# Kernel tuning notes

Hardware: AMD Instinct MI355X
Metric: run time of the kernel (lower is better)

## Reference

```python
import jax, jax.numpy as jnp
import numpy as np

N_NODES = 100000
N_EDGES = 600000
IN_FEATS = 128
HIDDEN = 128


def sage_conv(x, src, dst, w_l, b_l, w_r, num_nodes):
    """PyG SAGEConv with mean aggregation.
    out = mean_{j in N(i)} x_j @ w_l.T + b_l + x_i @ w_r.T
    src/dst: int arrays [E]; messages flow src -> dst.
    """
    msgs = x[src]                                             # [E, F] gather
    summed = jax.ops.segment_sum(msgs, dst, num_segments=num_nodes)  # [N, F]
    ones = jnp.ones((src.shape[0],), dtype=x.dtype)
    deg = jax.ops.segment_sum(ones, dst, num_segments=num_nodes)     # [N]
    agg = summed / jnp.maximum(deg, 1.0)[:, None]             # mean, safe for deg=0
    return agg @ w_l.T + b_l + x @ w_r.T


def setup_inputs() -> dict:
    key = jax.random.key(0)
    ks = jax.random.split(key, 10)

    def glorot(k, shape):
        fan_in = shape[-1]
        bound = 1.0 / np.sqrt(fan_in)
        return jax.random.uniform(k, shape, jnp.float32, -bound, bound)

    x = jax.random.normal(ks[0], (N_NODES, IN_FEATS), dtype=jnp.float32)
    xedge = jax.random.randint(ks[1], (2, N_EDGES), 0, N_NODES, dtype=jnp.int64)
    return {
        "x": x,
        "xedge": xedge,
        # SAGEConv 1 (in_feats -> hidden): lin_l (with bias) + lin_r (no bias)
        "w1_l": glorot(ks[2], (HIDDEN, IN_FEATS)),
        "b1_l": glorot(ks[3], (HIDDEN,)),
        "w1_r": glorot(ks[4], (HIDDEN, IN_FEATS)),
        # SAGEConv 2 (hidden -> hidden)
        "w2_l": glorot(ks[5], (HIDDEN, HIDDEN)),
        "b2_l": glorot(ks[6], (HIDDEN,)),
        "w2_r": glorot(ks[7], (HIDDEN, HIDDEN)),
        # Decoder: Linear(hidden -> hidden)
        "w_dec": glorot(ks[8], (HIDDEN, HIDDEN)),
        "b_dec": glorot(ks[9], (HIDDEN,)),
    }


def reference(x, xedge, w1_l, b1_l, w1_r, w2_l, b2_l, w2_r, w_dec, b_dec):
    src, dst = xedge[0], xedge[1]
    n = x.shape[0]
    h = sage_conv(x, src, dst, w1_l, b1_l, w1_r, n)   # conv1
    h = jax.nn.relu(h)
    # dropout omitted (deterministic eval semantics)
    h = sage_conv(h, src, dst, w2_l, b2_l, w2_r, n)   # conv2 -> encoder output
    dx = h @ w_dec.T + b_dec                          # decoder
    return (h, dx)
```

## Files before the change

kernel.cpp:

```cpp
#include <hip/hip_runtime.h>

typedef __attribute__((ext_vector_type(8))) short bf16x8;
typedef __attribute__((ext_vector_type(4))) float f32x4;
typedef unsigned int uint;
typedef unsigned short ushort;

#define NFEAT 128

__device__ __forceinline__ ushort f2b(float f) {
    uint u = __float_as_uint(f);
    u = (u + 0x7fffu + ((u >> 16) & 1u)) >> 16;
    return (ushort)u;
}

__device__ __forceinline__ void gload_lds16(const ushort* g, char* lds) {
    __builtin_amdgcn_global_load_lds((const __attribute__((address_space(1))) void*)g,
                                     (__attribute__((address_space(3))) void*)lds, 16, 0, 0);
}

__global__ __launch_bounds__(256) void prep(
    const float* __restrict__ x, ushort* __restrict__ x_bf, long nx,
    const float* __restrict__ w1l, const float* __restrict__ w1r,
    const float* __restrict__ w2l, const float* __restrict__ w2r,
    const float* __restrict__ wd,
    ushort* __restrict__ wc1, ushort* __restrict__ wc2, ushort* __restrict__ wdec,
    const int* __restrict__ dst, int* __restrict__ deg, int E, int nCvt)
{
    const int b = blockIdx.x;
    if (b < nCvt) {
        long i = ((long)b * 256 + threadIdx.x) * 4;
        if (i < nx) {
            float4 v = *(const float4*)(x + i);
            ushort4 o;
            o.x = f2b(v.x); o.y = f2b(v.y); o.z = f2b(v.z); o.w = f2b(v.w);
            *(ushort4*)(x_bf + i) = o;
        }
    } else if (b < nCvt + 256) {
        const int bb = b - nCvt;
        const int i = (bb & 127) * 256 + threadIdx.x;
        const int row = i >> 8, col = i & 255;
        const float* wl = (bb < 128) ? w1l : w2l;
        const float* wr = (bb < 128) ? w1r : w2r;
        ushort* dstw = (bb < 128) ? wc1 : wc2;
        float v = (col < 128) ? wl[row * 128 + col] : wr[row * 128 + col - 128];
        dstw[i] = f2b(v);
    } else if (b < nCvt + 320) {
        const int i = (b - nCvt - 256) * 256 + threadIdx.x;
        wdec[i] = f2b(wd[i]);
    } else {
        const int e = (b - nCvt - 320) * 256 + threadIdx.x;
        if (e < E) atomicAdd(&deg[dst[e]], 1);
    }
}

__global__ __launch_bounds__(256) void scan_blocks(const int* __restrict__ in, int* __restrict__ out,
                                                   int* __restrict__ bsum, int n) {
    __shared__ int lds[256];
    const int t = threadIdx.x;
    const int base = blockIdx.x * 1024 + t * 4;
    int a[4];
#pragma unroll
    for (int q = 0; q < 4; ++q) a[q] = (base + q < n) ? in[base + q] : 0;
    const int tsum = a[0] + a[1] + a[2] + a[3];
    lds[t] = tsum;
    __syncthreads();
    for (int off = 1; off < 256; off <<= 1) {
        int v = (t >= off) ? lds[t - off] : 0;
        __syncthreads();
        lds[t] += v;
        __syncthreads();
    }
    const int excl = lds[t] - tsum;
    if (t == 255) bsum[blockIdx.x] = lds[255];
    int r = excl;
#pragma unroll
    for (int q = 0; q < 4; ++q) {
        if (base + q < n) out[base + q] = r;
        r += a[q];
    }
}

__global__ __launch_bounds__(256) void scan_add(int* __restrict__ row_off, int* __restrict__ pos,
                                                const int* __restrict__ bsum, int n, int E) {
    const int i = blockIdx.x * 256 + threadIdx.x;
    const int cb = blockIdx.x >> 2;
    const int lane = threadIdx.x & 63;
    int v = 0;
    if (lane < cb) v += bsum[lane];
    if (lane + 64 < cb) v += bsum[lane + 64];
#pragma unroll
    for (int off = 1; off < 64; off <<= 1) v += __shfl_xor(v, off);
    if (i < n) {
        const int r = row_off[i] + v;
        row_off[i] = r;
        pos[i] = r;
    }
    if (i == 0) row_off[n] = E;
}

__global__ void fill_csr(const int* __restrict__ src, const int* __restrict__ dst,
                         int* __restrict__ pos, int* __restrict__ perm, int E) {
    const int e = blockIdx.x * blockDim.x + threadIdx.x;
    if (e < E) {
        const int p = atomicAdd(&pos[dst[e]], 1);
        perm[p] = src[e];
    }
}

__global__ __launch_bounds__(256) void gather_mean_bf(const int* __restrict__ row_off,
                                                      const int* __restrict__ perm,
                                                      const ushort* __restrict__ feat,
                                                      ushort* __restrict__ out, int n) {
    const int node = (blockIdx.x * 256 + threadIdx.x) >> 4;
    if (node >= n) return;
    const int chunk = threadIdx.x & 15;
    const int lo = row_off[node], hi = row_off[node + 1];
    float acc[8] = {0.f, 0.f, 0.f, 0.f, 0.f, 0.f, 0.f, 0.f};
    const uint4 z = make_uint4(0, 0, 0, 0);
    for (int i = lo; i < hi; i += 4) {
        const int rem = hi - i;
        const int s0 = perm[i];
        const int s1 = perm[(rem > 1) ? i + 1 : i];
        const int s2 = perm[(rem > 2) ? i + 2 : i];
        const int s3 = perm[(rem > 3) ? i + 3 : i];
        uint4 v0 = *(const uint4*)(feat + (size_t)s0 * NFEAT + chunk * 8);
        uint4 v1 = *(const uint4*)(feat + (size_t)s1 * NFEAT + chunk * 8);
        uint4 v2 = *(const uint4*)(feat + (size_t)s2 * NFEAT + chunk * 8);
        uint4 v3 = *(const uint4*)(feat + (size_t)s3 * NFEAT + chunk * 8);
        if (rem < 2) v1 = z;
        if (rem < 3) v2 = z;
        if (rem < 4) v3 = z;
        const uint p0[4] = {v0.x, v0.y, v0.z, v0.w};
        const uint p1[4] = {v1.x, v1.y, v1.z, v1.w};
        const uint p2[4] = {v2.x, v2.y, v2.z, v2.w};
        const uint p3[4] = {v3.x, v3.y, v3.z, v3.w};
#pragma unroll
        for (int q = 0; q < 4; ++q) {
            acc[2 * q]     += __uint_as_float(p0[q] << 16) + __uint_as_float(p1[q] << 16)
                            + __uint_as_float(p2[q] << 16) + __uint_as_float(p3[q] << 16);
            acc[2 * q + 1] += __uint_as_float(p0[q] & 0xffff0000u) + __uint_as_float(p1[q] & 0xffff0000u)
                            + __uint_as_float(p2[q] & 0xffff0000u) + __uint_as_float(p3[q] & 0xffff0000u);
        }
    }
    const float inv = 1.0f / fmaxf((float)(hi - lo), 1.0f);
    ushort o[8] __attribute__((aligned(16)));
#pragma unroll
    for (int q = 0; q < 8; ++q) o[q] = f2b(acc[q] * inv);
    *(uint4*)(out + (size_t)node * NFEAT + chunk * 8) = *(const uint4*)o;
}

template <bool RELU, bool DEC>
__global__ __launch_bounds__(256) void sage_mfma(
    const ushort* __restrict__ Amean, const ushort* __restrict__ Axin,
    const ushort* __restrict__ Wcat, const float* __restrict__ bias,
    const ushort* __restrict__ Wdec, const float* __restrict__ bdec,
    float* __restrict__ outf, ushort* __restrict__ outb,
    float* __restrict__ dxp, int n)
{
    __shared__ uint4 smem4[1536];
    char* As = (char*)smem4;
    char* Ws = As + 8192;
    const int t = threadIdx.x;
    const int m0 = blockIdx.x * 64;
    const int lane = t & 63;
    const int wid = t >> 6;
    const int lrow = lane & 15;
    const int lq = lane >> 4;

    f32x4 acc[8];
#pragma unroll
    for (int nn = 0; nn < 8; ++nn) acc[nn] = (f32x4){0.f, 0.f, 0.f, 0.f};

    for (int kt = 0; kt < 4; ++kt) {
        const ushort* Abase = (kt < 2) ? Amean : Axin;
        const int co = (kt & 1) * 64;
#pragma unroll
        for (int i = 0; i < 2; ++i) {
            const int row = i * 32 + wid * 8 + (lane >> 3);
            const int c = (lane & 7) ^ (row & 7);
            int gm = m0 + row;
            if (gm >= n) gm = n - 1;
            gload_lds16(Abase + (size_t)gm * NFEAT + co + c * 8,
                        As + i * 4096 + wid * 1024);
        }
#pragma unroll
        for (int i = 0; i < 4; ++i) {
            const int row = i * 32 + wid * 8 + (lane >> 3);
            const int c = (lane & 7) ^ (row & 7);
            gload_lds16(Wcat + (size_t)row * 256 + kt * 64 + c * 8,
                        Ws + i * 4096 + wid * 1024);
        }
        __syncthreads();
#pragma unroll
        for (int ks = 0; ks < 2; ++ks) {
            bf16x8 af, bfr[8];
            {
                const int row = wid * 16 + lrow;
                af = *(const bf16x8*)(As + row * 128 + (((ks * 4 + lq) * 16) ^ ((row & 7) << 4)));
            }
#pragma unroll
            for (int nn = 0; nn < 8; ++nn) {
                const int row = nn * 16 + lrow;
                bfr[nn] = *(const bf16x8*)(Ws + row * 128 + (((ks * 4 + lq) * 16) ^ ((row & 7) << 4)));
            }
#pragma unroll
            for (int nn = 0; nn < 8; ++nn)
                acc[nn] = __builtin_amdgcn_mfma_f32_16x16x32_bf16(bfr[nn], af, acc[nn], 0, 0, 0);
        }
        __syncthreads();
    }

    char* Lh = As;
    const int row = wid * 16 + lrow;
    const int grow = m0 + row;
#pragma unroll
    for (int nn = 0; nn < 8; ++nn) {
        const int colb = nn * 16 + lq * 4;
        const float4 bv = *(const float4*)(bias + colb);
        float v0 = acc[nn][0] + bv.x;
        float v1 = acc[nn][1] + bv.y;
        float v2 = acc[nn][2] + bv.z;
        float v3 = acc[nn][3] + bv.w;
        if (RELU) {
            v0 = fmaxf(v0, 0.f); v1 = fmaxf(v1, 0.f);
            v2 = fmaxf(v2, 0.f); v3 = fmaxf(v3, 0.f);
        }
        ushort4 ob;
        ob.x = f2b(v0); ob.y = f2b(v1); ob.z = f2b(v2); ob.w = f2b(v3);
        if (grow < n) {
            if (outf) *(float4*)(outf + (size_t)grow * NFEAT + colb) = make_float4(v0, v1, v2, v3);
            if (outb) *(ushort4*)(outb + (size_t)grow * NFEAT + colb) = ob;
        }
        if (DEC)
            *(ushort4*)(Lh + row * 256 + ((colb * 2) ^ ((row & 7) << 4))) = ob;
    }
    if (DEC) {
        f32x4 acc2[8];
#pragma unroll
        for (int nn = 0; nn < 8; ++nn) acc2[nn] = (f32x4){0.f, 0.f, 0.f, 0.f};
#pragma unroll
        for (int ks = 0; ks < 4; ++ks) {
            bf16x8 af2, bf2[8];
            af2 = *(const bf16x8*)(Lh + row * 256 + ((ks * 64 + lq * 16) ^ ((row & 7) << 4)));
#pragma unroll
            for (int nn = 0; nn < 8; ++nn)
                bf2[nn] = *(const bf16x8*)(Wdec + (size_t)(nn * 16 + lrow) * NFEAT + ks * 32 + lq * 8);
#pragma unroll
            for (int nn = 0; nn < 8; ++nn)
                acc2[nn] = __builtin_amdgcn_mfma_f32_16x16x32_bf16(bf2[nn], af2, acc2[nn], 0, 0, 0);
        }
        if (grow < n) {
#pragma unroll
            for (int nn = 0; nn < 8; ++nn) {
                const int colb = nn * 16 + lq * 4;
                const float4 bv = *(const float4*)(bdec + colb);
                *(float4*)(dxp + (size_t)grow * NFEAT + colb) =
                    make_float4(acc2[nn][0] + bv.x, acc2[nn][1] + bv.y,
                                acc2[nn][2] + bv.z, acc2[nn][3] + bv.w);
            }
        }
    }
}

extern "C" void kernel_launch(void* const* d_in, const int* in_sizes, int n_in,
                              void* d_out, int out_size, void* d_ws, size_t ws_size,
                              hipStream_t stream) {
    const float* x     = (const float*)d_in[0];
    const int*   xedge = (const int*)d_in[1];
    const float* w1_l  = (const float*)d_in[2];
    const float* b1_l  = (const float*)d_in[3];
    const float* w1_r  = (const float*)d_in[4];
    const float* w2_l  = (const float*)d_in[5];
    const float* b2_l  = (const float*)d_in[6];
    const float* w2_r  = (const float*)d_in[7];
    const float* w_dec = (const float*)d_in[8];
    const float* b_dec = (const float*)d_in[9];

    const int N = in_sizes[0] / NFEAT;
    const int E = in_sizes[1] / 2;
    const int* src = xedge;
    const int* dst = xedge + E;

    float* h_out = (float*)d_out;
    float* dxp   = h_out + (size_t)N * NFEAT;

    char* ws = (char*)d_ws;
    ushort* x_bf    = (ushort*)ws;
    ushort* h1_bf   = x_bf   + (size_t)N * NFEAT;
    ushort* mean_bf = h1_bf  + (size_t)N * NFEAT;
    ushort* wc1     = mean_bf + (size_t)N * NFEAT;
    ushort* wc2     = wc1 + 128 * 256;
    ushort* wdec    = wc2 + 128 * 256;
    int* deg        = (int*)(wdec + 128 * 128);
    int* row_off    = deg + N;
    int* pos        = row_off + (N + 1);
    int* bsum       = pos + N;
    int* perm       = bsum + 256;

    hipMemsetAsync(deg, 0, (size_t)N * sizeof(int), stream);
    const long nx = (long)N * NFEAT;
    const int nCvt = (int)((nx / 4 + 255) / 256);
    const int histB = (E + 255) / 256;
    prep<<<nCvt + 320 + histB, 256, 0, stream>>>(x, x_bf, nx, w1_l, w1_r, w2_l, w2_r, w_dec,
                                                 wc1, wc2, wdec, dst, deg, E, nCvt);

    const int nb = (N + 1023) / 1024;
    scan_blocks<<<nb, 256, 0, stream>>>(deg, row_off, bsum, N);
    scan_add<<<(N + 255) / 256, 256, 0, stream>>>(row_off, pos, bsum, N, E);
    fill_csr<<<histB, 256, 0, stream>>>(src, dst, pos, perm, E);

    const int gb = (N + 63) / 64;
    const int ggb = (N * 16 + 255) / 256;

    gather_mean_bf<<<ggb, 256, 0, stream>>>(row_off, perm, x_bf, mean_bf, N);
    sage_mfma<true, false><<<gb, 256, 0, stream>>>(mean_bf, x_bf, wc1, b1_l,
                                                   nullptr, nullptr, nullptr, h1_bf, nullptr, N);

    gather_mean_bf<<<ggb, 256, 0, stream>>>(row_off, perm, h1_bf, mean_bf, N);
    sage_mfma<false, true><<<gb, 256, 0, stream>>>(mean_bf, h1_bf, wc2, b2_l,
                                                   wdec, b_dec, h_out, nullptr, dxp, N);

    (void)n_in; (void)out_size; (void)ws_size;
}
```

Before: 201.8 us.

## Replace two-pass scan with decoupled lookback scan and widen gather unroll

Merges the block scan and the add pass into one decoupled-lookback prefix scan, so one kernel launch and one pass over row offsets go away. hipMemsetAsync is replaced by small zeroing kernels for the degree and lookback state arrays. The neighbour gather now loads eight indices and rows per iteration instead of four, to get more loads in flight. Lookback depends on all blocks being resident, and the wider unroll raises register use.

```diff
diff --git a/kernel.cpp b/kernel.cpp
--- a/kernel.cpp
+++ b/kernel.cpp
@@ -16,6 +16,11 @@
 __device__ __forceinline__ void gload_lds16(const ushort* g, char* lds) {
     __builtin_amdgcn_global_load_lds((const __attribute__((address_space(1))) void*)g,
                                      (__attribute__((address_space(3))) void*)lds, 16, 0, 0);
+}
+
+__global__ __launch_bounds__(256) void zero_kernel(int* __restrict__ p, int n4) {
+    const int i = blockIdx.x * 256 + threadIdx.x;
+    if (i < n4) *(int4*)(p + i * 4) = make_int4(0, 0, 0, 0);
 }
 
 __global__ __launch_bounds__(256) void prep(
@@ -53,14 +58,17 @@
     }
 }
 
-__global__ __launch_bounds__(256) void scan_blocks(const int* __restrict__ in, int* __restrict__ out,
-                                                   int* __restrict__ bsum, int n) {
+__global__ __launch_bounds__(256) void scan_lookback(
+    const int* __restrict__ deg, int* __restrict__ row_off, int* __restrict__ pos,
+    int* __restrict__ state, int n, int E)
+{
     __shared__ int lds[256];
-    const int t = threadIdx.x;
-    const int base = blockIdx.x * 1024 + t * 4;
+    __shared__ int sExcl;
+    const int b = blockIdx.x, t = threadIdx.x;
+    const int base = b * 1024 + t * 4;
     int a[4];
 #pragma unroll
-    for (int q = 0; q < 4; ++q) a[q] = (base + q < n) ? in[base + q] : 0;
+    for (int q = 0; q < 4; ++q) a[q] = (base + q < n) ? deg[base + q] : 0;
     const int tsum = a[0] + a[1] + a[2] + a[3];
     lds[t] = tsum;
     __syncthreads();
@@ -70,32 +78,35 @@
         lds[t] += v;
         __syncthreads();
     }
-    const int excl = lds[t] - tsum;
-    if (t == 255) bsum[blockIdx.x] = lds[255];
-    int r = excl;
+    const int texcl = lds[t] - tsum;
+    const int total = lds[255];
+    if (t == 0) {
+        if (b == 0) {
+            __hip_atomic_store(&state[0], (total << 2) | 2, __ATOMIC_RELEASE, __HIP_MEMORY_SCOPE_AGENT);
+            sExcl = 0;
+        } else {
+            __hip_atomic_store(&state[b], (total << 2) | 1, __ATOMIC_RELEASE, __HIP_MEMORY_SCOPE_AGENT);
+            int ex = 0;
+            for (int j = b - 1; j >= 0; --j) {
+                int s;
+                do {
+                    s = __hip_atomic_load(&state[j], __ATOMIC_ACQUIRE, __HIP_MEMORY_SCOPE_AGENT);
+                } while ((s & 3) == 0);
+                ex += s >> 2;
+                if ((s & 3) == 2) break;
+            }
+            __hip_atomic_store(&state[b], ((ex + total) << 2) | 2, __ATOMIC_RELEASE, __HIP_MEMORY_SCOPE_AGENT);
+            sExcl = ex;
+        }
+    }
+    __syncthreads();
+    int r = sExcl + texcl;
 #pragma unroll
     for (int q = 0; q < 4; ++q) {
-        if (base + q < n) out[base + q] = r;
+        if (base + q < n) { row_off[base + q] = r; pos[base + q] = r; }
         r += a[q];
     }
-}
-
-__global__ __launch_bounds__(256) void scan_add(int* __restrict__ row_off, int* __restrict__ pos,
-                                                const int* __restrict__ bsum, int n, int E) {
-    const int i = blockIdx.x * 256 + threadIdx.x;
-    const int cb = blockIdx.x >> 2;
-    const int lane = threadIdx.x & 63;
-    int v = 0;
-    if (lane < cb) v += bsum[lane];
-    if (lane + 64 < cb) v += bsum[lane + 64];
-#pragma unroll
-    for (int off = 1; off < 64; off <<= 1) v += __shfl_xor(v, off);
-    if (i < n) {
-        const int r = row_off[i] + v;
-        row_off[i] = r;
-        pos[i] = r;
-    }
-    if (i == 0) row_off[n] = E;
+    if (b == 0 && t == 0) row_off[n] = E;
 }
 
 __global__ void fill_csr(const int* __restrict__ src, const int* __restrict__ dst,
@@ -114,32 +125,27 @@
     const int node = (blockIdx.x * 256 + threadIdx.x) >> 4;
     if (node >= n) return;
     const int chunk = threadIdx.x & 15;
+    const ushort* fp = feat + chunk * 8;
     const int lo = row_off[node], hi = row_off[node + 1];
     float acc[8] = {0.f, 0.f, 0.f, 0.f, 0.f, 0.f, 0.f, 0.f};
     const uint4 z = make_uint4(0, 0, 0, 0);
-    for (int i = lo; i < hi; i += 4) {
-        const int rem = hi - i;
-        const int s0 = perm[i];
-        const int s1 = perm[(rem > 1) ? i + 1 : i];
-        const int s2 = perm[(rem > 2) ? i + 2 : i];
-        const int s3 = perm[(rem > 3) ? i + 3 : i];
-        uint4 v0 = *(const uint4*)(feat + (size_t)s0 * NFEAT + chunk * 8);
-        uint4 v1 = *(const uint4*)(feat + (size_t)s1 * NFEAT + chunk * 8);
-        uint4 v2 = *(const uint4*)(feat + (size_t)s2 * NFEAT + chunk * 8);
-        uint4 v3 = *(const uint4*)(feat + (size_t)s3 * NFEAT + chunk * 8);
-        if (rem < 2) v1 = z;
-        if (rem < 3) v2 = z;
-        if (rem < 4) v3 = z;
-        const uint p0[4] = {v0.x, v0.y, v0.z, v0.w};
-        const uint p1[4] = {v1.x, v1.y, v1.z, v1.w};
-        const uint p2[4] = {v2.x, v2.y, v2.z, v2.w};
-        const uint p3[4] = {v3.x, v3.y, v3.z, v3.w};
-#pragma unroll
-        for (int q = 0; q < 4; ++q) {
-            acc[2 * q]     += __uint_as_float(p0[q] << 16) + __uint_as_float(p1[q] << 16)
-                            + __uint_as_float(p2[q] << 16) + __uint_as_float(p3[q] << 16);
-            acc[2 * q + 1] += __uint_as_float(p0[q] & 0xffff0000u) + __uint_as_float(p1[q] & 0xffff0000u)
-                            + __uint_as_float(p2[q] & 0xffff0000u) + __uint_as_float(p3[q] & 0xffff0000u);
+    for (int i = lo; i < hi; i += 8) {
+        int idx[8];
+#pragma unroll
+        for (int k = 0; k < 8; ++k) idx[k] = perm[(i + k < hi) ? i + k : i];
+        uint4 v[8];
+#pragma unroll
+        for (int k = 0; k < 8; ++k) v[k] = *(const uint4*)(fp + (size_t)idx[k] * NFEAT);
+#pragma unroll
+        for (int k = 0; k < 8; ++k) if (i + k >= hi) v[k] = z;
+#pragma unroll
+        for (int k = 0; k < 8; ++k) {
+            const uint p[4] = {v[k].x, v[k].y, v[k].z, v[k].w};
+#pragma unroll
+            for (int q = 0; q < 4; ++q) {
+                acc[2 * q]     += __uint_as_float(p[q] << 16);
+                acc[2 * q + 1] += __uint_as_float(p[q] & 0xffff0000u);
+            }
         }
     }
     const float inv = 1.0f / fmaxf((float)(hi - lo), 1.0f);
@@ -294,19 +300,25 @@
     int* deg        = (int*)(wdec + 128 * 128);
     int* row_off    = deg + N;
     int* pos        = row_off + (N + 1);
-    int* bsum       = pos + N;
-    int* perm       = bsum + 256;
-
-    hipMemsetAsync(deg, 0, (size_t)N * sizeof(int), stream);
+    int* state      = pos + N;
+    int* perm       = state + 512;
+
+    const int nb = (N + 1023) / 1024;
+
+    {
+        const int degi4 = (N + 3) / 4;
+        const int sti4  = 512 / 4;
+        zero_kernel<<<(degi4 + 255) / 256, 256, 0, stream>>>(deg, degi4);
+        zero_kernel<<<(sti4 + 255) / 256, 256, 0, stream>>>(state, sti4);
+    }
+
     const long nx = (long)N * NFEAT;
     const int nCvt = (int)((nx / 4 + 255) / 256);
     const int histB = (E + 255) / 256;
     prep<<<nCvt + 320 + histB, 256, 0, stream>>>(x, x_bf, nx, w1_l, w1_r, w2_l, w2_r, w_dec,
                                                  wc1, wc2, wdec, dst, deg, E, nCvt);
 
-    const int nb = (N + 1023) / 1024;
-    scan_blocks<<<nb, 256, 0, stream>>>(deg, row_off, bsum, N);
-    scan_add<<<(N + 255) / 256, 256, 0, stream>>>(row_off, pos, bsum, N, E);
+    scan_lookback<<<nb, 256, 0, stream>>>(deg, row_off, pos, state, N, E);
     fill_csr<<<histB, 256, 0, stream>>>(src, dst, pos, perm, E);
 
     const int gb = (N + 63) / 64;
```

Result: slower. 217.5 us (+7.8%).
